# Optimization experiments

Hardware: AMD Instinct MI355X
Metric: run time of the kernel (lower is better)

Reference implementation:

```python
import math
import jax, jax.numpy as jnp
import numpy as np

B, T, C, H = 8, 1024, 768, 12
HD = C // H


def setup_inputs() -> dict:
    key = jax.random.key(0)
    ks = jax.random.split(key, 6)
    x = jax.random.normal(ks[0], (B, T, C), dtype=jnp.float32)
    # causal mask with right-padding: first half of batch full causal,
    # second half has last 128 key positions invalid
    causal = jnp.tril(jnp.ones((T, T), dtype=bool))  # [T,T]
    key_valid = jnp.ones((B, T), dtype=bool)
    key_valid = key_valid.at[B // 2:, T - 128:].set(False)
    mask = causal[None, None, :, :] & key_valid[:, None, None, :]  # [B,1,T,T]
    query_mask = key_valid[:, None, :, None]  # [B,1,T,1]
    s = 0.02
    W_attn = jax.random.normal(ks[1], (C, 3 * C), dtype=jnp.float32) * s
    b_attn = jax.random.normal(ks[2], (3 * C,), dtype=jnp.float32) * s
    W_proj = jax.random.normal(ks[3], (C, C), dtype=jnp.float32) * s
    b_proj = jax.random.normal(ks[4], (C,), dtype=jnp.float32) * s
    return {"x": x, "mask": mask, "query_mask": query_mask,
            "W_attn": W_attn, "b_attn": b_attn,
            "W_proj": W_proj, "b_proj": b_proj}


def reference(x, mask, query_mask, W_attn, b_attn, W_proj, b_proj):
    b, t, c = x.shape
    qkv = x @ W_attn + b_attn                      # [b,t,3c]
    q, k, v = jnp.split(qkv, 3, axis=-1)
    q = q.reshape(b, t, H, HD).transpose(0, 2, 1, 3)  # [b,h,t,d]
    k = k.reshape(b, t, H, HD).transpose(0, 2, 1, 3)
    v = v.reshape(b, t, H, HD).transpose(0, 2, 1, 3)
    att = jnp.einsum('bhqd,bhkd->bhqk', q, k) / math.sqrt(HD)
    neg_inf = jnp.finfo(att.dtype).min
    att = jnp.where(mask, att, -jnp.inf)
    no_valid_keys = ~jnp.any(mask, axis=-1, keepdims=True)  # [b,1,t,1]
    att = jnp.where(no_valid_keys, 0.0, att)
    att = jax.nn.softmax(att, axis=-1)
    qm = query_mask.astype(att.dtype)              # [b,1,t,1]
    att = att * qm
    out = jnp.einsum('bhqk,bhkd->bhqd', att, v)    # [b,h,t,d]
    out = out * qm
    out = jnp.where(no_valid_keys, 0.0, out)
    out = out.transpose(0, 2, 1, 3).reshape(b, t, c)
    return out @ W_proj + b_proj
```

## Files before the change

kernel.cpp:

```cpp
#include <hip/hip_runtime.h>
#include <hip/hip_bf16.h>
#include <stdint.h>

#define Bdim 8
#define Tdim 1024
#define Cdim 768
#define Hdim 12
#define HDdim 64
#define NROW (Bdim*Tdim)

typedef __attribute__((ext_vector_type(8))) short s16x8;
typedef __attribute__((ext_vector_type(8))) unsigned short u16x8;
typedef __attribute__((ext_vector_type(4))) unsigned short u16x4;
typedef __attribute__((ext_vector_type(4))) float f32x4;

__device__ __forceinline__ unsigned short f2bf(float f) {
  union { float f; uint32_t u; } c; c.f = f;
  uint32_t r = (c.u + 0x7FFFu + ((c.u >> 16) & 1u)) >> 16;
  return (unsigned short)r;
}
__device__ __forceinline__ unsigned short cvt_bf16(float f) {
  union { __hip_bfloat16 h; unsigned short u; } c;
  c.h = __float2bfloat16(f);
  return c.u;
}
__device__ __forceinline__ float exp2_hw(float x) {
  float r; asm("v_exp_f32 %0, %1" : "=v"(r) : "v"(x)); return r;
}
__device__ __forceinline__ void gload16(const void* g, void* l) {
  __builtin_amdgcn_global_load_lds(
      (const __attribute__((address_space(1))) unsigned int*)g,
      (__attribute__((address_space(3))) unsigned int*)l, 16, 0, 0);
}

__global__ __launch_bounds__(256) void mask_parse(const void* __restrict__ qm,
                                                  float* __restrict__ kvb) {
  unsigned w0 = *(const unsigned*)qm;
  int idx = blockIdx.x * 256 + threadIdx.x;
  bool v;
  if (w0 == 0x01010101u)       v = ((const unsigned char*)qm)[idx] != 0;
  else if (w0 == 0x3F800000u)  v = ((const float*)qm)[idx] != 0.f;
  else                         v = ((const int*)qm)[idx] != 0;
  kvb[idx] = v ? 0.f : -1e30f;
}

__global__ __launch_bounds__(256) void cvt_f32_bf16(const float* __restrict__ in,
                                                    unsigned short* __restrict__ out,
                                                    int n) {
  int i = (blockIdx.x * 256 + threadIdx.x) * 4;
  if (i + 3 < n) {
    float4 v = *(const float4*)&in[i];
    out[i+0] = f2bf(v.x); out[i+1] = f2bf(v.y);
    out[i+2] = f2bf(v.z); out[i+3] = f2bf(v.w);
  }
}

__global__ __launch_bounds__(256) void transpose_cvt(const float* __restrict__ in,
                                                     unsigned short* __restrict__ out,
                                                     int K, int N) {
  __shared__ float tile[32][33];
  int n0 = blockIdx.x * 32, k0 = blockIdx.y * 32;
  int tx = threadIdx.x, ty = threadIdx.y;
  #pragma unroll
  for (int i = 0; i < 4; i++)
    tile[ty + i*8][tx] = in[(size_t)(k0 + ty + i*8) * N + n0 + tx];
  __syncthreads();
  #pragma unroll
  for (int i = 0; i < 4; i++)
    out[(size_t)(n0 + ty + i*8) * K + k0 + tx] = f2bf(tile[tx][ty + i*8]);
}

__global__ __launch_bounds__(256) void vtrans(const unsigned short* __restrict__ Vi,
                                              unsigned short* __restrict__ Vo) {
  __shared__ unsigned short tile[64][72];
  int t0 = blockIdx.x * 64;
  int bh = blockIdx.y;
  const unsigned short* src = Vi + (size_t)bh * Tdim * 64;
  unsigned short* dst = Vo + (size_t)bh * 64 * Tdim;
  int tid = threadIdx.x;
  int r = tid >> 3, c8 = (tid & 7) * 8;
  #pragma unroll
  for (int p = 0; p < 2; p++)
    *(u16x8*)&tile[p*32 + r][c8] = *(const u16x8*)&src[(size_t)(t0 + p*32 + r) * 64 + c8];
  __syncthreads();
  #pragma unroll
  for (int p = 0; p < 2; p++) {
    int d = p*32 + r;
    u16x8 o;
    #pragma unroll
    for (int j = 0; j < 8; j++) o[j] = tile[c8 + j][d];
    *(u16x8*)&dst[(size_t)d * Tdim + t0 + c8] = o;
  }
}

template<int MODE, int BM>
__global__ __launch_bounds__(256, 2) void gemm_bt(
    const unsigned short* __restrict__ A,
    const unsigned short* __restrict__ BT,
    const float* __restrict__ bias,
    unsigned short* __restrict__ Qo, unsigned short* __restrict__ Ko,
    unsigned short* __restrict__ Vo,
    float* __restrict__ Out) {
  __shared__ unsigned short As[2][BM * 32];
  __shared__ unsigned short Bs[2][128 * 32];
  constexpr int WR = BM / 2;
  constexpr int MF = WR / 16;
  constexpr int XB = 1024 / BM;
  const int K = 768;
  const int NK = K / 32;
  int lin = blockIdx.y * gridDim.x + blockIdx.x;
  int xcd = lin & 7, jj = lin >> 3;
  int bx = xcd * XB + (jj & (XB - 1));
  int by = jj / XB;
  int m0 = bx * BM, n0 = by * 128;
  int tid = threadIdx.x;
  int lane = tid & 63, wv = tid >> 6;
  int wr = wv >> 1, wc = wv & 1;
  int l16 = lane & 15, g = lane >> 4;
  f32x4 acc[MF][4];
  #pragma unroll
  for (int m = 0; m < MF; m++)
    #pragma unroll
    for (int n = 0; n < 4; n++) acc[m][n] = (f32x4){0.f, 0.f, 0.f, 0.f};

  int o = tid * 16;
  int r0 = o >> 6;
  int kb2 = (o & 63) >> 1;

  #pragma unroll
  for (int i = 0; i < BM/64; i++)
    gload16(&A[(size_t)(m0 + i*64 + r0) * K + kb2], (char*)As[0] + i*4096 + o);
  gload16(&BT[(size_t)(n0 +      r0) * K + kb2], (char*)Bs[0] + o);
  gload16(&BT[(size_t)(n0 + 64 + r0) * K + kb2], (char*)Bs[0] + 4096 + o);

  for (int kt = 0; kt < NK; kt++) {
    const int cur = kt & 1;
    __syncthreads();
    if (kt + 1 < NK) {
      int k0 = (kt + 1) * 32;
      #pragma unroll
      for (int i = 0; i < BM/64; i++)
        gload16(&A[(size_t)(m0 + i*64 + r0) * K + k0 + kb2], (char*)As[cur^1] + i*4096 + o);
      gload16(&BT[(size_t)(n0 +      r0) * K + k0 + kb2], (char*)Bs[cur^1] + o);
      gload16(&BT[(size_t)(n0 + 64 + r0) * K + k0 + kb2], (char*)Bs[cur^1] + 4096 + o);
    }
    s16x8 af[MF], bfr[4];
    #pragma unroll
    for (int m = 0; m < MF; m++)
      af[m] = *(const s16x8*)((const char*)As[cur] + ((wr*WR + m*16 + l16) * 64 + g*16));
    #pragma unroll
    for (int n = 0; n < 4; n++)
      bfr[n] = *(const s16x8*)((const char*)Bs[cur] + ((wc*64 + n*16 + l16) * 64 + g*16));
    #pragma unroll
    for (int m = 0; m < MF; m++)
      #pragma unroll
      for (int n = 0; n < 4; n++)
        acc[m][n] = __builtin_amdgcn_mfma_f32_16x16x32_bf16(af[m], bfr[n], acc[m][n], 0, 0, 0);
  }

  #pragma unroll
  for (int m = 0; m < MF; m++) {
    int row = m0 + wr*WR + m*16 + g*4;
    #pragma unroll
    for (int n = 0; n < 4; n++) {
      int col = n0 + wc*64 + n*16 + l16;
      float bv = bias[col];
      #pragma unroll
      for (int q = 0; q < 4; q++) {
        float v = acc[m][n][q] + bv;
        int rr = row + q;
        if (MODE == 0) {
          int which = col / 768;
          int cc = col - which * 768;
          int hh = cc >> 6, d = cc & 63;
          int bb = rr >> 10, t = rr & 1023;
          size_t dst = (((size_t)bb * Hdim + hh) * Tdim + t) * HDdim + d;
          if (which == 0)      Qo[dst] = f2bf(v * 0.18033688011112042f);
          else if (which == 1) Ko[dst] = f2bf(v);
          else                 Vo[dst] = f2bf(v);
        } else {
          Out[(size_t)rr * 768 + col] = v;
        }
      }
    }
  }
}

__device__ __forceinline__ void stage_issue(const unsigned short* kh,
                                            const unsigned short* vh,
                                            int kv0, int row, int c8,
                                            u16x8* kreg, u16x8* vreg) {
  kreg[0] = *(const u16x8*)&kh[(size_t)(kv0 + row) * 64 + c8];
  kreg[1] = *(const u16x8*)&kh[(size_t)(kv0 + 32 + row) * 64 + c8];
  vreg[0] = *(const u16x8*)&vh[(size_t)row * Tdim + kv0 + c8];
  vreg[1] = *(const u16x8*)&vh[(size_t)(32 + row) * Tdim + kv0 + c8];
}
__device__ __forceinline__ void stage_commit(unsigned short* Ksb, unsigned short* Vsb,
                                             int row, int c8,
                                             const u16x8* kreg, const u16x8* vreg) {
  int swz = (row & 7) << 4;
  *(u16x8*)((char*)Ksb + (((     row)*128 + c8*2) ^ swz)) = kreg[0];
  *(u16x8*)((char*)Ksb + (((32 + row)*128 + c8*2) ^ swz)) = kreg[1];
  *(u16x8*)((char*)Vsb + (((     row)*128 + c8*2) ^ swz)) = vreg[0];
  *(u16x8*)((char*)Vsb + (((32 + row)*128 + c8*2) ^ swz)) = vreg[1];
}

__global__ __launch_bounds__(256, 3) void attn_mfma(
    const unsigned short* __restrict__ Qb,
    const unsigned short* __restrict__ Kb,
    const unsigned short* __restrict__ Vt,
    const float* __restrict__ kvb,
    unsigned short* __restrict__ attout) {
  __shared__ unsigned short Ks[2][64 * 64];
  __shared__ unsigned short Vs[2][64 * 64];
  __shared__ unsigned short Ps[4][16 * 64];

  const int f = blockIdx.x;
  const int zp = f / 96;
  const int hb = f - zp * 96;
  const int h = hb % Hdim, b = hb / Hdim;
  const int tid = threadIdx.x;
  const int lane = tid & 63, w = tid >> 6;
  const int l16 = lane & 15, g = lane >> 4;
  const size_t head = ((size_t)b * Hdim + h) * Tdim;
  const unsigned short* qh = Qb + head * 64;
  const unsigned short* kh = Kb + head * 64;
  const unsigned short* vh = Vt + head * 64;
  const float* kvr = kvb + b * Tdim;
  const int swz = (l16 & 7) << 4;
  char* myP = (char*)Ps[w];
  const int srow = tid >> 3, sc8 = (tid & 7) * 8;

  u16x8 kreg[2], vreg[2];

  for (int ph = 0; ph < 2; ph++) {
    const int myTile = ph ? (15 - zp) : zp;
    const int q0w = myTile * 64 + w * 16;
    const int nkv = myTile + 1;
    const int qg = q0w + l16;

    s16x8 qf0 = *(const s16x8*)&qh[(size_t)qg * 64 + g*8];
    s16x8 qf1 = *(const s16x8*)&qh[(size_t)qg * 64 + 32 + g*8];

    float m_r = -1e30f, l_r = 0.f;
    f32x4 oacc[4];
    #pragma unroll
    for (int nt = 0; nt < 4; nt++) oacc[nt] = (f32x4){0.f, 0.f, 0.f, 0.f};

    stage_issue(kh, vh, 0, srow, sc8, kreg, vreg);
    stage_commit(Ks[0], Vs[0], srow, sc8, kreg, vreg);
    if (nkv > 1) stage_issue(kh, vh, 64, srow, sc8, kreg, vreg);
    __syncthreads();

    for (int kt = 0; kt < nkv; kt++) {
      const int buf = kt & 1;
      const int kv0 = kt * 64;
      const unsigned short* Ksb = Ks[buf];
      const unsigned short* Vsb = Vs[buf];

      f32x4 st[4];
      #pragma unroll
      for (int it = 0; it < 4; it++) st[it] = (f32x4){0.f, 0.f, 0.f, 0.f};
      #pragma unroll
      for (int kc = 0; kc < 2; kc++) {
        s16x8 kf[4];
        #pragma unroll
        for (int it = 0; it < 4; it++)
          kf[it] = *(const s16x8*)((const char*)Ksb +
                     (((it*16 + l16)*128 + kc*64 + g*16) ^ swz));
        __builtin_amdgcn_s_setprio(1);
        #pragma unroll
        for (int it = 0; it < 4; it++)
          st[it] = __builtin_amdgcn_mfma_f32_16x16x32_bf16(kf[it], kc ? qf1 : qf0, st[it], 0, 0, 0);
        __builtin_amdgcn_s_setprio(0);
      }

      const bool isdiag = (kt == myTile);
      float pm = -1e30f;
      #pragma unroll
      for (int it = 0; it < 4; it++) {
        float4 kb4 = *(const float4*)&kvr[kv0 + it*16 + g*4];
        #pragma unroll
        for (int reg = 0; reg < 4; reg++) {
          float s = st[it][reg] + ((const float*)&kb4)[reg];
          if (isdiag) {
            int kg = kv0 + it*16 + g*4 + reg;
            s = (kg <= qg) ? s : -1e30f;
          }
          st[it][reg] = s;
          pm = fmaxf(pm, s);
        }
      }
      pm = fmaxf(pm, __shfl_xor(pm, 16));
      pm = fmaxf(pm, __shfl_xor(pm, 32));

      if (!__all(pm - m_r <= 8.f)) {
        float mnew = fmaxf(m_r, pm);
        float sc = exp2_hw(m_r - mnew);
        m_r = mnew;
        l_r *= sc;
        #pragma unroll
        for (int reg = 0; reg < 4; reg++) {
          float s2 = __shfl(sc, (lane & 48) | (g*4 + reg));
          #pragma unroll
          for (int nt = 0; nt < 4; nt++) oacc[nt][reg] *= s2;
        }
      }

      float psum = 0.f;
      u16x4 pw[4];
      #pragma unroll
      for (int it = 0; it < 4; it++)
        #pragma unroll
        for (int reg = 0; reg < 4; reg++) {
          float p = exp2_hw(st[it][reg] - m_r);
          psum += p;
          pw[it][reg] = cvt_bf16(p);
        }
      psum += __shfl_xor(psum, 16);
      psum += __shfl_xor(psum, 32);
      l_r += psum;
      #pragma unroll
      for (int it = 0; it < 4; it++)
        *(u16x4*)(myP + ((l16*128 + it*32 + g*8) ^ swz)) = pw[it];

      #pragma unroll
      for (int kc = 0; kc < 2; kc++) {
        s16x8 pa = *(const s16x8*)(myP + ((l16*128 + kc*64 + g*16) ^ swz));
        s16x8 vf[4];
        #pragma unroll
        for (int nt = 0; nt < 4; nt++)
          vf[nt] = *(const s16x8*)((const char*)Vsb +
                     (((nt*16 + l16)*128 + kc*64 + g*16) ^ swz));
        __builtin_amdgcn_s_setprio(1);
        #pragma unroll
        for (int nt = 0; nt < 4; nt++)
          oacc[nt] = __builtin_amdgcn_mfma_f32_16x16x32_bf16(pa, vf[nt], oacc[nt], 0, 0, 0);
        __builtin_amdgcn_s_setprio(0);
      }

      if (kt + 1 < nkv) {
        stage_commit(Ks[(kt+1)&1], Vs[(kt+1)&1], srow, sc8, kreg, vreg);
        if (kt + 2 < nkv) stage_issue(kh, vh, (kt+2)*64, srow, sc8, kreg, vreg);
      }
      __syncthreads();
    }

    float qbias = kvr[qg];
    float iv = (qbias == 0.f && l_r > 0.f) ? (1.f / l_r) : 0.f;
    #pragma unroll
    for (int reg = 0; reg < 4; reg++) {
      float ivv = __shfl(iv, (lane & 48) | (g*4 + reg));
      int qq = q0w + g*4 + reg;
      unsigned short* op = &attout[(size_t)(b * Tdim + qq) * 768 + h * 64];
      #pragma unroll
      for (int nt = 0; nt < 4; nt++)
        op[nt*16 + l16] = f2bf(oacc[nt][reg] * ivv);
    }
  }
}

extern "C" void kernel_launch(void* const* d_in, const int* in_sizes, int n_in,
                              void* d_out, int out_size, void* d_ws, size_t ws_size,
                              hipStream_t stream) {
  const float* x  = (const float*)d_in[0];
  const void*  qmask = d_in[2];
  const float* Wa = (const float*)d_in[3];
  const float* ba = (const float*)d_in[4];
  const float* Wp = (const float*)d_in[5];
  const float* bp = (const float*)d_in[6];
  float* out = (float*)d_out;

  char* ws = (char*)d_ws;
  unsigned short* xb   = (unsigned short*)(ws + 0);
  unsigned short* WaT  = (unsigned short*)(ws + 12582912);
  unsigned short* WpT  = (unsigned short*)(ws + 16121856);
  unsigned short* Qb   = (unsigned short*)(ws + 17301504);
  unsigned short* Kb   = (unsigned short*)(ws + 29884416);
  unsigned short* Vb   = (unsigned short*)(ws + 42467328);
  unsigned short* Ab   = (unsigned short*)(ws + 55050240);
  float*          kvb  = (float*)(ws + 67633152);

  unsigned short* Vtmp = Ab;

  mask_parse<<<32, 256, 0, stream>>>(qmask, kvb);
  cvt_f32_bf16<<<6144, 256, 0, stream>>>(x, xb, NROW * 768);
  transpose_cvt<<<dim3(72, 24), dim3(32, 8), 0, stream>>>(Wa, WaT, 768, 2304);
  transpose_cvt<<<dim3(24, 24), dim3(32, 8), 0, stream>>>(Wp, WpT, 768, 768);
  gemm_bt<0,128><<<dim3(64, 18), 256, 0, stream>>>(xb, WaT, ba, Qb, Kb, Vtmp, nullptr);
  vtrans<<<dim3(16, 96), 256, 0, stream>>>(Vtmp, Vb);
  attn_mfma<<<768, 256, 0, stream>>>(Qb, Kb, Vb, kvb, Ab);
  gemm_bt<1,64><<<dim3(128, 6), 256, 0, stream>>>(Ab, WpT, bp, nullptr, nullptr, nullptr, out);
}
```

Before: 131.2 us.

## Triple-buffer GEMM shared-memory tiles with explicit vmcnt waits and prefetch distance two

Moves the bias GEMM's LDS staging from double to triple buffering. It issues loads two k-tiles ahead and replaces __syncthreads with explicit s_waitcnt vmcnt counts plus a raw barrier, so more global-to-LDS traffic stays in flight. Occupancy is raised to 3 blocks per CU through launch bounds. This uses more LDS per block, which may limit occupancy. The hardcoded vmcnt values assume a fixed number of loads per stage for each MODE, and correctness depends on that assumption.

```diff
diff --git a/kernel.cpp b/kernel.cpp
--- a/kernel.cpp
+++ b/kernel.cpp
@@ -94,15 +94,15 @@
 }
 
 template<int MODE, int BM>
-__global__ __launch_bounds__(256, 2) void gemm_bt(
+__global__ __launch_bounds__(256, 3) void gemm_bt(
     const unsigned short* __restrict__ A,
     const unsigned short* __restrict__ BT,
     const float* __restrict__ bias,
     unsigned short* __restrict__ Qo, unsigned short* __restrict__ Ko,
     unsigned short* __restrict__ Vo,
     float* __restrict__ Out) {
-  __shared__ unsigned short As[2][BM * 32];
-  __shared__ unsigned short Bs[2][128 * 32];
+  __shared__ unsigned short As[3][BM * 32];
+  __shared__ unsigned short Bs[3][128 * 32];
   constexpr int WR = BM / 2;
   constexpr int MF = WR / 16;
   constexpr int XB = 1024 / BM;
@@ -127,30 +127,39 @@
   int r0 = o >> 6;
   int kb2 = (o & 63) >> 1;
 
-  #pragma unroll
-  for (int i = 0; i < BM/64; i++)
-    gload16(&A[(size_t)(m0 + i*64 + r0) * K + kb2], (char*)As[0] + i*4096 + o);
-  gload16(&BT[(size_t)(n0 +      r0) * K + kb2], (char*)Bs[0] + o);
-  gload16(&BT[(size_t)(n0 + 64 + r0) * K + kb2], (char*)Bs[0] + 4096 + o);
+  auto issue = [&](int kt) {
+    int k0 = kt * 32;
+    int slot = kt % 3;
+    #pragma unroll
+    for (int i = 0; i < BM/64; i++)
+      gload16(&A[(size_t)(m0 + i*64 + r0) * K + k0 + kb2], (char*)As[slot] + i*4096 + o);
+    gload16(&BT[(size_t)(n0 +      r0) * K + k0 + kb2], (char*)Bs[slot] + o);
+    gload16(&BT[(size_t)(n0 + 64 + r0) * K + k0 + kb2], (char*)Bs[slot] + 4096 + o);
+  };
+
+  issue(0);
+  issue(1);
 
   for (int kt = 0; kt < NK; kt++) {
-    const int cur = kt & 1;
-    __syncthreads();
     if (kt + 1 < NK) {
-      int k0 = (kt + 1) * 32;
-      #pragma unroll
-      for (int i = 0; i < BM/64; i++)
-        gload16(&A[(size_t)(m0 + i*64 + r0) * K + k0 + kb2], (char*)As[cur^1] + i*4096 + o);
-      gload16(&BT[(size_t)(n0 +      r0) * K + k0 + kb2], (char*)Bs[cur^1] + o);
-      gload16(&BT[(size_t)(n0 + 64 + r0) * K + k0 + kb2], (char*)Bs[cur^1] + 4096 + o);
+      if constexpr (MODE == 0) asm volatile("s_waitcnt vmcnt(4)" ::: "memory");
+      else                     asm volatile("s_waitcnt vmcnt(3)" ::: "memory");
+    } else {
+      asm volatile("s_waitcnt vmcnt(0)" ::: "memory");
     }
+    __builtin_amdgcn_s_barrier();
+    if (kt + 2 < NK) issue(kt + 2);
+
+    const int slot = kt % 3;
+    const char* Asb = (const char*)As[slot];
+    const char* Bsb = (const char*)Bs[slot];
     s16x8 af[MF], bfr[4];
     #pragma unroll
     for (int m = 0; m < MF; m++)
-      af[m] = *(const s16x8*)((const char*)As[cur] + ((wr*WR + m*16 + l16) * 64 + g*16));
+      af[m] = *(const s16x8*)(Asb + ((wr*WR + m*16 + l16) * 64 + g*16));
     #pragma unroll
     for (int n = 0; n < 4; n++)
-      bfr[n] = *(const s16x8*)((const char*)Bs[cur] + ((wc*64 + n*16 + l16) * 64 + g*16));
+      bfr[n] = *(const s16x8*)(Bsb + ((wc*64 + n*16 + l16) * 64 + g*16));
     #pragma unroll
     for (int m = 0; m < MF; m++)
       #pragma unroll
```

Result: faster. 126.7 us (-3.4%).
